# Performance work log

Measured on AMD Instinct MI355X. Metric: run time of the kernel, lower is better.

## Reference

```python
import jax, jax.numpy as jnp
import numpy as np

DM = 1024
N_HEADS = 16
DK = DM // N_HEADS
BS, SEQ = 4, 2048


def setup_inputs() -> dict:
    key = jax.random.key(0)
    k1, k2, k3 = jax.random.split(key, 3)
    scale = 1.0 / np.sqrt(DM)
    return {
        "x": jax.random.normal(k1, (BS, SEQ, DM), dtype=jnp.float32),
        "w_qkv": jax.random.normal(k2, (DM, 3 * DM), dtype=jnp.float32) * scale,
        "b_qkv": jnp.zeros((3 * DM,), dtype=jnp.float32),
        "w_out": jax.random.normal(k3, (DM, DM), dtype=jnp.float32) * scale,
        "b_out": jnp.zeros((DM,), dtype=jnp.float32),
    }


def reference(x, w_qkv, b_qkv, w_out, b_out):
    bs, seq_len, dm = x.shape
    qkv = x @ w_qkv + b_qkv                      # [bs, seq, 3*dm]
    q, k, v = jnp.split(qkv, 3, axis=-1)
    # [bs, heads, seq, dk]
    def heads(t):
        return t.reshape(bs, seq_len, N_HEADS, DK).transpose(0, 2, 1, 3)
    q, k, v = heads(q), heads(k), heads(v)
    w = jnp.einsum("bhqd,bhkd->bhqk", q, k) / np.sqrt(DK)
    causal = jnp.tril(jnp.ones((seq_len, seq_len), dtype=bool))
    w = jnp.where(causal, w, -jnp.inf)
    w = jax.nn.softmax(w, axis=-1)               # attn_dropout p=0 -> identity
    z = jnp.einsum("bhqk,bhkd->bhqd", w, v)
    z = z.transpose(0, 2, 1, 3).reshape(bs, seq_len, dm)
    return z @ w_out + b_out                     # resid_dropout p=0 -> identity
```

## Files before the change

### kernel.cpp

```cpp
#include <hip/hip_runtime.h>
#include <hip/hip_bf16.h>

typedef unsigned short u16;
typedef unsigned int u32;
typedef short bf16x8 __attribute__((ext_vector_type(8)));
typedef float f32x4 __attribute__((ext_vector_type(4)));

#define DM 1024
#define SEQ 2048
#define MTOK 8192
#define NQKV 3072

#define QSCALE 0.18033688011112042f

#define BAR() __builtin_amdgcn_s_barrier()
#define VMW(n) asm volatile("s_waitcnt vmcnt(" #n ")" ::: "memory")
#define LGKW() asm volatile("s_waitcnt lgkmcnt(0)" ::: "memory")

__device__ __forceinline__ u16 f2bf(float f) {
  union { float f; unsigned u; } a; a.f = f;
  unsigned r = a.u + 0x7FFFu + ((a.u >> 16) & 1u);
  return (u16)(r >> 16);
}

__device__ __forceinline__ u32 cvt2(float a, float b) {
  __hip_bfloat162 t = __float22bfloat162_rn(make_float2(a, b));
  u32 r; __builtin_memcpy(&r, &t, 4); return r;
}

__device__ __forceinline__ void gload_lds16(const u16* g, u16* l) {
  __builtin_amdgcn_global_load_lds(
      (const __attribute__((address_space(1))) unsigned int*)g,
      (__attribute__((address_space(3))) unsigned int*)l, 16, 0, 0);
}

__global__ __launch_bounds__(256) void cast_x_kernel(const float* __restrict__ in,
                                                     u16* __restrict__ out) {
  int i = blockIdx.x * 256 + threadIdx.x;
  float4 v = ((const float4*)in)[i];
  ushort4 o;
  o.x = f2bf(v.x); o.y = f2bf(v.y); o.z = f2bf(v.z); o.w = f2bf(v.w);
  ((ushort4*)out)[i] = o;
}

__global__ __launch_bounds__(256) void transpose_cast_kernel(const float* __restrict__ in,
                                                             u16* __restrict__ out,
                                                             int R, int C) {
  __shared__ float tile[32][33];
  const int tx = threadIdx.x & 31, ty = threadIdx.x >> 5;
  const int r0 = blockIdx.y << 5, c0 = blockIdx.x << 5;
#pragma unroll
  for (int i = 0; i < 32; i += 8)
    tile[ty + i][tx] = in[(size_t)(r0 + ty + i) * C + (c0 + tx)];
  __syncthreads();
#pragma unroll
  for (int i = 0; i < 32; i += 8)
    out[(size_t)(c0 + ty + i) * R + (r0 + tx)] = f2bf(tile[tx][ty + i]);
}

template <int EPI>
__global__ __launch_bounds__(256, 2) void gemm2_kernel(
    const u16* __restrict__ A, const u16* __restrict__ Bt,
    const float* __restrict__ bias,
    u16* __restrict__ oq, u16* __restrict__ ok, u16* __restrict__ ovT,
    float* __restrict__ of, int N) {
  __shared__ alignas(16) u16 As[2][128 * 64];
  __shared__ alignas(16) u16 Bs[2][128 * 64];

  const int tid = threadIdx.x, lane = tid & 63, wid = tid >> 6;
  const int wr = wid >> 1, wc = wid & 1;
  const int l15 = lane & 15, l4 = lane >> 4;
  const int swz = l15 & 7;

  const int xcd = blockIdx.x & 7, idx = blockIdx.x >> 3;
  const int row0 = ((xcd << 3) + (idx & 7)) << 7;
  const int col0 = (idx >> 3) << 7;

  const int sr = tid >> 3;
  const int scsw = ((tid & 7) ^ (sr & 7)) << 3;
  const u16* asrc = A + (size_t)(row0 + sr) * 1024 + scsw;
  const u16* bsrc = Bt + (size_t)(col0 + sr) * 1024 + scsw;

  auto stage = [&](int buf, int kt) {
#pragma unroll
    for (int j = 0; j < 4; ++j)
      gload_lds16(asrc + (size_t)(j << 5) * 1024 + (kt << 6),
                  &As[buf][0] + (j << 11) + tid * 8);
#pragma unroll
    for (int j = 0; j < 4; ++j)
      gload_lds16(bsrc + (size_t)(j << 5) * 1024 + (kt << 6),
                  &Bs[buf][0] + (j << 11) + tid * 8);
  };

  f32x4 acc[4][4];
#pragma unroll
  for (int m = 0; m < 4; ++m)
#pragma unroll
    for (int n = 0; n < 4; ++n) acc[m][n] = (f32x4){0.f, 0.f, 0.f, 0.f};

  stage(0, 0);
  stage(1, 1);

  int cur = 0;
#pragma unroll 1
  for (int t = 0; t < 16; ++t) {
    if (t < 15) { VMW(8); } else { VMW(0); }
    BAR();

    bf16x8 af[4][2], bfr[4][2];
    {
      const u16* base = &As[cur][0] + ((wr << 6) + l15) * 64;
#pragma unroll
      for (int mf = 0; mf < 4; ++mf)
#pragma unroll
        for (int ks = 0; ks < 2; ++ks)
          af[mf][ks] = *(const bf16x8*)(base + (mf << 4) * 64 + ((((ks << 2) + l4) ^ swz) << 3));
    }
    {
      const u16* base = &Bs[cur][0] + ((wc << 6) + l15) * 64;
#pragma unroll
      for (int nf = 0; nf < 4; ++nf)
#pragma unroll
        for (int ks = 0; ks < 2; ++ks)
          bfr[nf][ks] = *(const bf16x8*)(base + (nf << 4) * 64 + ((((ks << 2) + l4) ^ swz) << 3));
    }
    LGKW();
    BAR();
    if (t < 14) stage(cur, t + 2);

    __builtin_amdgcn_s_setprio(1);
#pragma unroll
    for (int ks = 0; ks < 2; ++ks)
#pragma unroll
      for (int mf = 0; mf < 4; ++mf)
#pragma unroll
        for (int nf = 0; nf < 4; ++nf)
          acc[mf][nf] = __builtin_amdgcn_mfma_f32_16x16x32_bf16(af[mf][ks], bfr[nf][ks],
                                                                acc[mf][nf], 0, 0, 0);
    __builtin_amdgcn_s_setprio(0);
    cur ^= 1;
  }

#pragma unroll
  for (int nf = 0; nf < 4; ++nf) {
    const int col = col0 + (wc << 6) + (nf << 4) + l15;
    const float bv = bias[col];
    if (EPI == 0) {
      const int sel = col >> 10;
      const int h = (col & 1023) >> 6;
      const int d = col & 63;
      const float scl = (sel == 0) ? QSCALE : 1.0f;
#pragma unroll
      for (int mf = 0; mf < 4; ++mf)
#pragma unroll
        for (int r = 0; r < 4; ++r) {
          const int row = row0 + (wr << 6) + (mf << 4) + (l4 << 2) + r;
          const int bb = row >> 11, s = row & 2047;
          const u16 v = f2bf((acc[mf][nf][r] + bv) * scl);
          const int bh = (bb << 4) + h;
          if (sel == 0)      oq[((size_t)bh * SEQ + s) * 64 + d] = v;
          else if (sel == 1) ok[((size_t)bh * SEQ + s) * 64 + d] = v;
          else               ovT[((size_t)bh * 64 + d) * SEQ + s] = v;
        }
    } else {
#pragma unroll
      for (int mf = 0; mf < 4; ++mf)
#pragma unroll
        for (int r = 0; r < 4; ++r) {
          const int row = row0 + (wr << 6) + (mf << 4) + (l4 << 2) + r;
          of[(size_t)row * N + col] = acc[mf][nf][r] + bv;
        }
    }
  }
}

__global__ __launch_bounds__(256, 4) void attn_kernel(const u16* __restrict__ qb,
                                                      const u16* __restrict__ kbuf,
                                                      const u16* __restrict__ vT,
                                                      u16* __restrict__ zb) {
  __shared__ alignas(16) u16 Ks[2][64 * 64];
  __shared__ alignas(16) u16 Vs[2][64 * 64];
  __shared__ alignas(16) u16 Ps[4][16 * 64];

  const int bid = blockIdx.x;
  const int xcd = bid & 7;
  const int idx = bid >> 3;
  const int bh = (xcd << 3) | (idx & 7);
  const int qpart = idx >> 3;
  const int qseg = 15 - qpart;
  const int b = bh >> 4, h = bh & 15;

  const int tid = threadIdx.x;
  const int lane = tid & 63, wid = tid >> 6;
  const int l15 = lane & 15, l4 = lane >> 4;
  const int swz = l15 & 7;

  const u16* qp = qb + (size_t)bh * SEQ * 64;
  const u16* kp = kbuf + (size_t)bh * SEQ * 64;
  const u16* vp = vT + (size_t)bh * 64 * SEQ;

  const int qw0 = (qseg << 7) + (wid << 5);
  const int nkt = (qseg + 1) << 1;
  const int ktmax = (qseg << 1) + (wid >> 1);

  const int srow = tid >> 3;
  const int schk = ((tid & 7) ^ (srow & 7)) << 3;
  const u16* ksrc = kp + (size_t)srow * 64 + schk;
  const u16* vsrc = vp + (size_t)srow * SEQ + schk;

  auto stage = [&](int buf, int kt) {
    gload_lds16(ksrc + (size_t)kt * 4096, &Ks[buf][0] + tid * 8);
    gload_lds16(ksrc + (size_t)kt * 4096 + 32 * 64, &Ks[buf][0] + 2048 + tid * 8);
    gload_lds16(vsrc + (size_t)kt * 64, &Vs[buf][0] + tid * 8);
    gload_lds16(vsrc + (size_t)kt * 64 + (size_t)32 * SEQ, &Vs[buf][0] + 2048 + tid * 8);
  };

  bf16x8 aq[2][2];
#pragma unroll
  for (int m = 0; m < 2; ++m)
#pragma unroll
    for (int c = 0; c < 2; ++c)
      aq[m][c] = *(const bf16x8*)(qp + (size_t)(qw0 + (m << 4) + l15) * 64 + (c << 5) + (l4 << 3));
  asm volatile("" :: "v"(aq[0][0]), "v"(aq[0][1]), "v"(aq[1][0]), "v"(aq[1][1]));

  const short osv = (short)0x3F80;
  const bf16x8 onesf = {osv, osv, osv, osv, osv, osv, osv, osv};

  f32x4 zo[2][5];
  float mrun[2] = {-INFINITY, -INFINITY};
#pragma unroll
  for (int m = 0; m < 2; ++m)
#pragma unroll
    for (int d = 0; d < 5; ++d) zo[m][d] = (f32x4){0.f, 0.f, 0.f, 0.f};

  u16* pw = &Ps[wid][0];

  stage(0, 0);
  stage(1, 1);

  int cur = 0;
#pragma unroll 1
  for (int kt = 0; kt < nkt; ++kt) {
    if (kt + 1 < nkt) { VMW(4); } else { VMW(0); }
    BAR();

    if (kt <= ktmax) {
      const int k0 = kt << 6;
      const u16* kb_ = &Ks[cur][0];
      const u16* vb_ = &Vs[cur][0];
      f32x4 s[2][4];
#pragma unroll
      for (int m = 0; m < 2; ++m)
#pragma unroll
        for (int nf = 0; nf < 4; ++nf) s[m][nf] = (f32x4){0.f, 0.f, 0.f, 0.f};
#pragma unroll
      for (int nf = 0; nf < 4; ++nf) {
        const u16* kr = kb_ + ((nf << 4) + l15) * 64;
        const bf16x8 kf0 = *(const bf16x8*)(kr + ((l4 ^ swz) << 3));
        const bf16x8 kf1 = *(const bf16x8*)(kr + (((l4 + 4) ^ swz) << 3));
#pragma unroll
        for (int m = 0; m < 2; ++m) {
          s[m][nf] = __builtin_amdgcn_mfma_f32_16x16x32_bf16(kf0, aq[m][0], s[m][nf], 0, 0, 0);
          s[m][nf] = __builtin_amdgcn_mfma_f32_16x16x32_bf16(kf1, aq[m][1], s[m][nf], 0, 0, 0);
        }
      }
      if (kt == ktmax) {
#pragma unroll
        for (int m = 0; m < 2; ++m) {
          const int qtok = qw0 + (m << 4) + l15;
#pragma unroll
          for (int nf = 0; nf < 4; ++nf)
#pragma unroll
            for (int r = 0; r < 4; ++r) {
              const int ktok = k0 + (nf << 4) + (l4 << 2) + r;
              if (ktok > qtok) s[m][nf][r] = -INFINITY;
            }
        }
      }
      bf16x8 pa[2][2];
#pragma unroll
      for (int m = 0; m < 2; ++m) {
        float mx = s[m][0][0];
#pragma unroll
        for (int nf = 0; nf < 4; ++nf)
#pragma unroll
          for (int r = 0; r < 4; ++r) mx = fmaxf(mx, s[m][nf][r]);
        mx = fmaxf(mx, __shfl_xor(mx, 16));
        mx = fmaxf(mx, __shfl_xor(mx, 32));
        if (__ballot(mx > mrun[m])) {
          const float mnew = fmaxf(mrun[m], mx);
          const float alpha = exp2f(mrun[m] - mnew);
          mrun[m] = mnew;
#pragma unroll
          for (int d = 0; d < 5; ++d) zo[m][d] *= alpha;
        }
#pragma unroll
        for (int nf = 0; nf < 4; ++nf) {
          f32x4 p;
#pragma unroll
          for (int r = 0; r < 4; ++r) p[r] = exp2f(s[m][nf][r] - mrun[m]);
          const int phys = ((nf << 1) + (l4 >> 1)) ^ swz;
          uint2 o; o.x = cvt2(p[0], p[1]); o.y = cvt2(p[2], p[3]);
          *(uint2*)(pw + l15 * 64 + phys * 8 + ((l4 & 1) << 2)) = o;
        }
#pragma unroll
        for (int c = 0; c < 2; ++c) {
          const int phys = ((c << 2) + l4) ^ swz;
          pa[m][c] = *(const bf16x8*)(pw + l15 * 64 + phys * 8);
        }
      }
#pragma unroll
      for (int d = 0; d < 4; ++d) {
        const u16* vr = vb_ + ((d << 4) + l15) * 64;
        const bf16x8 vf0 = *(const bf16x8*)(vr + ((l4 ^ swz) << 3));
        const bf16x8 vf1 = *(const bf16x8*)(vr + (((l4 + 4) ^ swz) << 3));
        zo[0][d] = __builtin_amdgcn_mfma_f32_16x16x32_bf16(vf0, pa[0][0], zo[0][d], 0, 0, 0);
        zo[0][d] = __builtin_amdgcn_mfma_f32_16x16x32_bf16(vf1, pa[0][1], zo[0][d], 0, 0, 0);
        zo[1][d] = __builtin_amdgcn_mfma_f32_16x16x32_bf16(vf0, pa[1][0], zo[1][d], 0, 0, 0);
        zo[1][d] = __builtin_amdgcn_mfma_f32_16x16x32_bf16(vf1, pa[1][1], zo[1][d], 0, 0, 0);
      }
      zo[0][4] = __builtin_amdgcn_mfma_f32_16x16x32_bf16(onesf, pa[0][0], zo[0][4], 0, 0, 0);
      zo[0][4] = __builtin_amdgcn_mfma_f32_16x16x32_bf16(onesf, pa[0][1], zo[0][4], 0, 0, 0);
      zo[1][4] = __builtin_amdgcn_mfma_f32_16x16x32_bf16(onesf, pa[1][0], zo[1][4], 0, 0, 0);
      zo[1][4] = __builtin_amdgcn_mfma_f32_16x16x32_bf16(onesf, pa[1][1], zo[1][4], 0, 0, 0);
    }

    BAR();
    if (kt + 2 < nkt) stage(cur, kt + 2);
    cur ^= 1;
  }

#pragma unroll
  for (int m = 0; m < 2; ++m) {
    const float inv = 1.0f / zo[m][4][0];
    const int q = qw0 + (m << 4) + l15;
#pragma unroll
    for (int d = 0; d < 4; ++d) {
      uint2 o;
      o.x = cvt2(zo[m][d][0] * inv, zo[m][d][1] * inv);
      o.y = cvt2(zo[m][d][2] * inv, zo[m][d][3] * inv);
      *(uint2*)(zb + (((size_t)b * SEQ + q) * 16 + h) * 64 + (d << 4) + (l4 << 2)) = o;
    }
  }
}

extern "C" void kernel_launch(void* const* d_in, const int* in_sizes, int n_in,
                              void* d_out, int out_size, void* d_ws, size_t ws_size,
                              hipStream_t stream) {
  const float* x     = (const float*)d_in[0];
  const float* w_qkv = (const float*)d_in[1];
  const float* b_qkv = (const float*)d_in[2];
  const float* w_out = (const float*)d_in[3];
  const float* b_out = (const float*)d_in[4];
  float* out = (float*)d_out;

  char* ws = (char*)d_ws;
  u16* xb    = (u16*)ws;  ws += (size_t)MTOK * DM * 2;
  u16* wqkvT = (u16*)ws;  ws += (size_t)NQKV * DM * 2;
  u16* woutT = (u16*)ws;  ws += (size_t)DM * DM * 2;
  u16* qb    = (u16*)ws;  ws += (size_t)MTOK * DM * 2;
  u16* kb    = (u16*)ws;  ws += (size_t)MTOK * DM * 2;
  u16* vTb   = (u16*)ws;  ws += (size_t)MTOK * DM * 2;
  u16* zbuf  = (u16*)ws;  ws += (size_t)MTOK * DM * 2;

  cast_x_kernel<<<MTOK * DM / 1024, 256, 0, stream>>>(x, xb);
  transpose_cast_kernel<<<dim3(NQKV / 32, DM / 32), 256, 0, stream>>>(w_qkv, wqkvT, DM, NQKV);
  transpose_cast_kernel<<<dim3(DM / 32, DM / 32), 256, 0, stream>>>(w_out, woutT, DM, DM);

  gemm2_kernel<0><<<1536, 256, 0, stream>>>(xb, wqkvT, b_qkv, qb, kb, vTb, nullptr, NQKV);

  attn_kernel<<<1024, 256, 0, stream>>>(qb, kb, vTb, zbuf);

  gemm2_kernel<1><<<512, 256, 0, stream>>>(zbuf, woutT, b_out, nullptr, nullptr, nullptr, out, DM);
}
```

Before: 197.6 us.

## Use atomic work-queue scheduling with 64-row query tiles in attention

New measurement: 373.9 us. 89.2% more time.

```diff
diff --git a/kernel.cpp b/kernel.cpp
--- a/kernel.cpp
+++ b/kernel.cpp
@@ -174,80 +174,87 @@
   }
 }
 
-__global__ __launch_bounds__(256, 4) void attn_kernel(const u16* __restrict__ qb,
+__global__ __launch_bounds__(128, 4) void attn_kernel(const u16* __restrict__ qb,
                                                       const u16* __restrict__ kbuf,
                                                       const u16* __restrict__ vT,
-                                                      u16* __restrict__ zb) {
+                                                      u16* __restrict__ zb,
+                                                      u32* __restrict__ counter) {
   __shared__ alignas(16) u16 Ks[2][64 * 64];
-  __shared__ alignas(16) u16 Vs[2][64 * 64];
-  __shared__ alignas(16) u16 Ps[4][16 * 64];
-
-  const int bid = blockIdx.x;
-  const int xcd = bid & 7;
-  const int idx = bid >> 3;
-  const int bh = (xcd << 3) | (idx & 7);
-  const int qpart = idx >> 3;
-  const int qseg = 15 - qpart;
-  const int b = bh >> 4, h = bh & 15;
+  __shared__ alignas(16) u16 Ps[2][16 * 64];
+  __shared__ u32 witem;
 
   const int tid = threadIdx.x;
   const int lane = tid & 63, wid = tid >> 6;
   const int l15 = lane & 15, l4 = lane >> 4;
   const int swz = l15 & 7;
 
-  const u16* qp = qb + (size_t)bh * SEQ * 64;
-  const u16* kp = kbuf + (size_t)bh * SEQ * 64;
-  const u16* vp = vT + (size_t)bh * 64 * SEQ;
-
-  const int qw0 = (qseg << 7) + (wid << 5);
-  const int nkt = (qseg + 1) << 1;
-  const int ktmax = (qseg << 1) + (wid >> 1);
-
   const int srow = tid >> 3;
   const int schk = ((tid & 7) ^ (srow & 7)) << 3;
-  const u16* ksrc = kp + (size_t)srow * 64 + schk;
-  const u16* vsrc = vp + (size_t)srow * SEQ + schk;
-
-  auto stage = [&](int buf, int kt) {
-    gload_lds16(ksrc + (size_t)kt * 4096, &Ks[buf][0] + tid * 8);
-    gload_lds16(ksrc + (size_t)kt * 4096 + 32 * 64, &Ks[buf][0] + 2048 + tid * 8);
-    gload_lds16(vsrc + (size_t)kt * 64, &Vs[buf][0] + tid * 8);
-    gload_lds16(vsrc + (size_t)kt * 64 + (size_t)32 * SEQ, &Vs[buf][0] + 2048 + tid * 8);
-  };
-
-  bf16x8 aq[2][2];
-#pragma unroll
-  for (int m = 0; m < 2; ++m)
-#pragma unroll
-    for (int c = 0; c < 2; ++c)
-      aq[m][c] = *(const bf16x8*)(qp + (size_t)(qw0 + (m << 4) + l15) * 64 + (c << 5) + (l4 << 3));
-  asm volatile("" :: "v"(aq[0][0]), "v"(aq[0][1]), "v"(aq[1][0]), "v"(aq[1][1]));
+  u16* pw = &Ps[wid][0];
 
   const short osv = (short)0x3F80;
   const bf16x8 onesf = {osv, osv, osv, osv, osv, osv, osv, osv};
 
-  f32x4 zo[2][5];
-  float mrun[2] = {-INFINITY, -INFINITY};
-#pragma unroll
-  for (int m = 0; m < 2; ++m)
-#pragma unroll
-    for (int d = 0; d < 5; ++d) zo[m][d] = (f32x4){0.f, 0.f, 0.f, 0.f};
-
-  u16* pw = &Ps[wid][0];
-
-  stage(0, 0);
-  stage(1, 1);
-
-  int cur = 0;
 #pragma unroll 1
-  for (int kt = 0; kt < nkt; ++kt) {
-    if (kt + 1 < nkt) { VMW(4); } else { VMW(0); }
-    BAR();
-
-    if (kt <= ktmax) {
+  for (;;) {
+    if (tid == 0) witem = atomicAdd(counter, 1u);
+    __syncthreads();
+    const u32 w = witem;
+    __syncthreads();
+    if (w >= 2048u) return;
+
+    const int j = 31 - (int)(w >> 6);
+    const int bh = (int)(w & 63u);
+    const int b = bh >> 4, h = bh & 15;
+
+    const u16* qp = qb + (size_t)bh * SEQ * 64;
+    const u16* kp = kbuf + (size_t)bh * SEQ * 64;
+    const u16* vp = vT + (size_t)bh * 64 * SEQ;
+    const u16* ksrc = kp + (size_t)srow * 64 + schk;
+
+    const int qw0 = (j << 6) + (wid << 5);
+    const int nkt = j + 1;
+
+    bf16x8 aq[2][2];
+#pragma unroll
+    for (int m = 0; m < 2; ++m)
+#pragma unroll
+      for (int c = 0; c < 2; ++c)
+        aq[m][c] = *(const bf16x8*)(qp + (size_t)(qw0 + (m << 4) + l15) * 64 + (c << 5) + (l4 << 3));
+    asm volatile("" :: "v"(aq[0][0]), "v"(aq[0][1]), "v"(aq[1][0]), "v"(aq[1][1]));
+
+    f32x4 zo[2][5];
+    float mrun[2] = {-INFINITY, -INFINITY};
+#pragma unroll
+    for (int m = 0; m < 2; ++m)
+#pragma unroll
+      for (int d = 0; d < 5; ++d) zo[m][d] = (f32x4){0.f, 0.f, 0.f, 0.f};
+
+    auto stage = [&](int buf, int kt) {
+#pragma unroll
+      for (int jj = 0; jj < 4; ++jj)
+        gload_lds16(ksrc + (size_t)kt * 4096 + (jj << 10),
+                    &Ks[buf][0] + (jj << 10) + tid * 8);
+    };
+
+    stage(0, 0);
+    stage(1, 1);
+
+    int cur = 0;
+#pragma unroll 1
+    for (int kt = 0; kt < nkt; ++kt) {
+      if (kt + 1 < nkt) { VMW(4); } else { VMW(0); }
+      BAR();
+
       const int k0 = kt << 6;
+      bf16x8 vf[4][2];
+#pragma unroll
+      for (int d = 0; d < 4; ++d) {
+        const u16* vr = vp + (size_t)((d << 4) + l15) * SEQ + k0 + (l4 << 3);
+        vf[d][0] = *(const bf16x8*)(vr);
+        vf[d][1] = *(const bf16x8*)(vr + 32);
+      }
       const u16* kb_ = &Ks[cur][0];
-      const u16* vb_ = &Vs[cur][0];
       f32x4 s[2][4];
 #pragma unroll
       for (int m = 0; m < 2; ++m)
@@ -264,7 +271,7 @@
           s[m][nf] = __builtin_amdgcn_mfma_f32_16x16x32_bf16(kf1, aq[m][1], s[m][nf], 0, 0, 0);
         }
       }
-      if (kt == ktmax) {
+      if (kt == nkt - 1) {
 #pragma unroll
         for (int m = 0; m < 2; ++m) {
           const int qtok = qw0 + (m << 4) + l15;
@@ -311,36 +318,34 @@
       }
 #pragma unroll
       for (int d = 0; d < 4; ++d) {
-        const u16* vr = vb_ + ((d << 4) + l15) * 64;
-        const bf16x8 vf0 = *(const bf16x8*)(vr + ((l4 ^ swz) << 3));
-        const bf16x8 vf1 = *(const bf16x8*)(vr + (((l4 + 4) ^ swz) << 3));
-        zo[0][d] = __builtin_amdgcn_mfma_f32_16x16x32_bf16(vf0, pa[0][0], zo[0][d], 0, 0, 0);
-        zo[0][d] = __builtin_amdgcn_mfma_f32_16x16x32_bf16(vf1, pa[0][1], zo[0][d], 0, 0, 0);
-        zo[1][d] = __builtin_amdgcn_mfma_f32_16x16x32_bf16(vf0, pa[1][0], zo[1][d], 0, 0, 0);
-        zo[1][d] = __builtin_amdgcn_mfma_f32_16x16x32_bf16(vf1, pa[1][1], zo[1][d], 0, 0, 0);
+        zo[0][d] = __builtin_amdgcn_mfma_f32_16x16x32_bf16(vf[d][0], pa[0][0], zo[0][d], 0, 0, 0);
+        zo[0][d] = __builtin_amdgcn_mfma_f32_16x16x32_bf16(vf[d][1], pa[0][1], zo[0][d], 0, 0, 0);
+        zo[1][d] = __builtin_amdgcn_mfma_f32_16x16x32_bf16(vf[d][0], pa[1][0], zo[1][d], 0, 0, 0);
+        zo[1][d] = __builtin_amdgcn_mfma_f32_16x16x32_bf16(vf[d][1], pa[1][1], zo[1][d], 0, 0, 0);
       }
       zo[0][4] = __builtin_amdgcn_mfma_f32_16x16x32_bf16(onesf, pa[0][0], zo[0][4], 0, 0, 0);
       zo[0][4] = __builtin_amdgcn_mfma_f32_16x16x32_bf16(onesf, pa[0][1], zo[0][4], 0, 0, 0);
       zo[1][4] = __builtin_amdgcn_mfma_f32_16x16x32_bf16(onesf, pa[1][0], zo[1][4], 0, 0, 0);
       zo[1][4] = __builtin_amdgcn_mfma_f32_16x16x32_bf16(onesf, pa[1][1], zo[1][4], 0, 0, 0);
-    }
-
-    BAR();
-    if (kt + 2 < nkt) stage(cur, kt + 2);
-    cur ^= 1;
-  }
-
-#pragma unroll
-  for (int m = 0; m < 2; ++m) {
-    const float inv = 1.0f / zo[m][4][0];
-    const int q = qw0 + (m << 4) + l15;
-#pragma unroll
-    for (int d = 0; d < 4; ++d) {
-      uint2 o;
-      o.x = cvt2(zo[m][d][0] * inv, zo[m][d][1] * inv);
-      o.y = cvt2(zo[m][d][2] * inv, zo[m][d][3] * inv);
-      *(uint2*)(zb + (((size_t)b * SEQ + q) * 16 + h) * 64 + (d << 4) + (l4 << 2)) = o;
-    }
+
+      BAR();
+      if (kt + 2 < nkt) stage(cur, kt + 2);
+      cur ^= 1;
+    }
+
+#pragma unroll
+    for (int m = 0; m < 2; ++m) {
+      const float inv = 1.0f / zo[m][4][0];
+      const int q = qw0 + (m << 4) + l15;
+#pragma unroll
+      for (int d = 0; d < 4; ++d) {
+        uint2 o;
+        o.x = cvt2(zo[m][d][0] * inv, zo[m][d][1] * inv);
+        o.y = cvt2(zo[m][d][2] * inv, zo[m][d][3] * inv);
+        *(uint2*)(zb + (((size_t)b * SEQ + q) * 16 + h) * 64 + (d << 4) + (l4 << 2)) = o;
+      }
+    }
+    __syncthreads();
   }
 }
 
@@ -362,6 +367,9 @@
   u16* kb    = (u16*)ws;  ws += (size_t)MTOK * DM * 2;
   u16* vTb   = (u16*)ws;  ws += (size_t)MTOK * DM * 2;
   u16* zbuf  = (u16*)ws;  ws += (size_t)MTOK * DM * 2;
+  u32* counter = (u32*)ws;
+
+  hipMemsetAsync(counter, 0, 4, stream);
 
   cast_x_kernel<<<MTOK * DM / 1024, 256, 0, stream>>>(x, xb);
   transpose_cast_kernel<<<dim3(NQKV / 32, DM / 32), 256, 0, stream>>>(w_qkv, wqkvT, DM, NQKV);
@@ -369,7 +377,7 @@
 
   gemm2_kernel<0><<<1536, 256, 0, stream>>>(xb, wqkvT, b_qkv, qb, kb, vTb, nullptr, NQKV);
 
-  attn_kernel<<<1024, 256, 0, stream>>>(qb, kb, vTb, zbuf);
+  attn_kernel<<<2048, 128, 0, stream>>>(qb, kb, vTb, zbuf, counter);
 
   gemm2_kernel<1><<<512, 256, 0, stream>>>(zbuf, woutT, b_out, nullptr, nullptr, nullptr, out, DM);
 }
```
